# Performance work log

Measured on AMD Instinct MI355X. Metric: run time of the kernel, lower is better.

The kernel has to match this reference:

```python
import jax, jax.numpy as jnp
import numpy as np

N_USERS = 100000
N_ITEMS = 50000
N_TOPICS = 1000
N_NODES = N_USERS + N_ITEMS + N_TOPICS
DIM = 64
LAYERS = 3
NNZ = 4000000
BATCH = 16384


def setup_inputs() -> dict:
    key = jax.random.key(0)
    ks = jax.random.split(key, 8)
    user_w = jax.random.normal(ks[0], (N_USERS, DIM), dtype=jnp.float32) * 0.1
    item_w = jax.random.normal(ks[1], (N_ITEMS, DIM), dtype=jnp.float32) * 0.1
    topic_w = jax.random.normal(ks[2], (N_TOPICS, DIM), dtype=jnp.float32) * 0.1
    vals = jax.random.uniform(ks[3], (NNZ,), dtype=jnp.float32)
    row = jax.random.randint(ks[4], (NNZ,), 0, N_NODES, dtype=jnp.int32)
    col = jax.random.randint(ks[5], (NNZ,), 0, N_NODES, dtype=jnp.int32)
    users = jax.random.randint(ks[6], (BATCH,), 0, N_USERS, dtype=jnp.int32)
    items = jax.random.randint(ks[7], (BATCH,), 0, N_ITEMS, dtype=jnp.int32)
    return {"user_w": user_w, "item_w": item_w, "topic_w": topic_w,
            "vals": vals, "row": row, "col": col,
            "users": users, "items": items}


def _spmm(vals, row, col, x):
    # y[r] = sum over edges e with row[e]==r of vals[e] * x[col[e]]
    msgs = vals[:, None] * x[col]  # [NNZ, DIM]
    return jax.ops.segment_sum(msgs, row, num_segments=N_NODES)


def reference(user_w, item_w, topic_w, vals, row, col, users, items):
    all_emb = jnp.concatenate([user_w, item_w, topic_w], axis=0)  # [N, D]
    acc = all_emb
    emb = all_emb
    for _ in range(LAYERS):
        emb = _spmm(vals, row, col, emb)
        acc = acc + emb
    out = acc / jnp.asarray(LAYERS + 1, dtype=acc.dtype)  # mean over stacked layers
    u = out[users]                       # [B, D] user rows
    i = out[N_USERS + items]             # [B, D] item rows (offset into node table)
    return jnp.sum(u * i, axis=1)        # [B]
```

## Files before the change

kernel.cpp:

```cpp
#include <hip/hip_runtime.h>
#include <hip/hip_fp16.h>

#define N_USERS 100000
#define N_ITEMS 50000
#define N_TOPICS 1000
#define N_NODES (N_USERS + N_ITEMS + N_TOPICS)
#define DIM 64
#define NNZ 4000000
#define BATCH 16384

#define BROWS 128
#define NB ((N_NODES + BROWS - 1) / BROWS)
#define NPART 512
#define CHUNK ((NNZ + NPART - 1) / NPART)
#define SEGCAP 4608

#define QSCALE 16384.0f
#define QINV   6.103515625e-05f

__global__ void concat_init(const float4* __restrict__ uw,
                            const float4* __restrict__ iw,
                            const float4* __restrict__ tw,
                            __half2* __restrict__ x0) {
    int tid = blockIdx.x * blockDim.x + threadIdx.x;
    const int total = N_NODES * (DIM / 4);
    if (tid >= total) return;
    int node = tid >> 4;
    int q = tid & 15;
    float4 v;
    if (node < N_USERS)                v = uw[node * 16 + q];
    else if (node < N_USERS + N_ITEMS) v = iw[(node - N_USERS) * 16 + q];
    else                               v = tw[(node - N_USERS - N_ITEMS) * 16 + q];
    x0[tid * 2]     = __floats2half2_rn(v.x, v.y);
    x0[tid * 2 + 1] = __floats2half2_rn(v.z, v.w);
}

__global__ void __launch_bounds__(1024)
part_count(const int* __restrict__ row, int* __restrict__ hcnt) {
    __shared__ int h[NB];
    const int g = blockIdx.x;
    const int t = threadIdx.x;
    for (int i = t; i < NB; i += 1024) h[i] = 0;
    __syncthreads();
    int e0 = g * CHUNK;
    int e1 = e0 + CHUNK; if (e1 > NNZ) e1 = NNZ;
    for (int e = e0 + t; e < e1; e += 1024) {
        int r = __builtin_nontemporal_load(&row[e]);
        atomicAdd(&h[r >> 7], 1);
    }
    __syncthreads();
    int* dst = hcnt + (size_t)g * NB;
    for (int i = t; i < NB; i += 1024) dst[i] = h[i];
}

__global__ void part_scanA(int* __restrict__ hcnt, int* __restrict__ bcnt) {
    int b = blockIdx.x * 4 + (threadIdx.x >> 6);
    int lane = threadIdx.x & 63;
    if (b >= NB) return;
    int carry = 0;
    for (int base = 0; base < NPART; base += 64) {
        int g = base + lane;
        int v = hcnt[(size_t)g * NB + b];
        int x = v;
        #pragma unroll
        for (int off = 1; off < 64; off <<= 1) {
            int y = __shfl_up(x, off, 64);
            if (lane >= off) x += y;
        }
        int tot = __shfl(x, 63, 64);
        hcnt[(size_t)g * NB + b] = carry + x - v;
        carry += tot;
    }
    if (lane == 0) bcnt[b] = carry;
}

__global__ void part_scanB(const int* __restrict__ bcnt,
                           int* __restrict__ bptr,
                           int* __restrict__ rowptr) {
    __shared__ int wsum[16];
    __shared__ int carry_s;
    const int t = threadIdx.x;
    const int lane = t & 63;
    const int wid = t >> 6;
    if (t == 0) carry_s = 0;
    __syncthreads();
    for (int base = 0; base < NB; base += 1024) {
        int i = base + t;
        int v = (i < NB) ? bcnt[i] : 0;
        int x = v;
        #pragma unroll
        for (int off = 1; off < 64; off <<= 1) {
            int y = __shfl_up(x, off, 64);
            if (lane >= off) x += y;
        }
        if (lane == 63) wsum[wid] = x;
        __syncthreads();
        int wbase = 0;
        for (int w = 0; w < wid; ++w) wbase += wsum[w];
        int excl = carry_s + wbase + (x - v);
        if (i < NB) bptr[i] = excl;
        __syncthreads();
        if (t == 1023) carry_s = excl + v;
        __syncthreads();
    }
    if (t == 0) { bptr[NB] = NNZ; rowptr[N_NODES] = NNZ; }
}

__global__ void __launch_bounds__(1024)
part_scatter(const int* __restrict__ row,
             const int* __restrict__ col,
             const float* __restrict__ vals,
             const int* __restrict__ hcnt,
             const int* __restrict__ bptr,
             int2* __restrict__ cvtmp) {
    __shared__ int cur[NB];
    const int g = blockIdx.x;
    const int t = threadIdx.x;
    const int* hoff = hcnt + (size_t)g * NB;
    for (int i = t; i < NB; i += 1024) cur[i] = bptr[i] + hoff[i];
    __syncthreads();
    int e0 = g * CHUNK;
    int e1 = e0 + CHUNK; if (e1 > NNZ) e1 = NNZ;
    for (int e = e0 + t; e < e1; e += 1024) {
        int r = __builtin_nontemporal_load(&row[e]);
        int c = __builtin_nontemporal_load(&col[e]);
        float v = __builtin_nontemporal_load(&vals[e]);
        int p = atomicAdd(&cur[r >> 7], 1);
        cvtmp[p] = make_int2(((r & (BROWS - 1)) << 18) | c, __float_as_int(v));
    }
}

__global__ void __launch_bounds__(256)
bucket_sort(const int* __restrict__ bptr,
            const long long* __restrict__ cvtmp,
            unsigned int* __restrict__ cv,
            int* __restrict__ rowptr) {
    __shared__ int2 seg[SEGCAP];
    __shared__ int cnt[BROWS];
    __shared__ int cur[BROWS];
    const int t = threadIdx.x;
    const int b = blockIdx.x;
    const int beg = bptr[b];
    const int end = bptr[b + 1];
    const int n = end - beg;

    for (int i = t; i < BROWS; i += 256) cnt[i] = 0;
    const bool lds_path = (n <= SEGCAP);

    if (lds_path) {
        for (int j = t; j < n; j += 256) {
            long long e = __builtin_nontemporal_load(&cvtmp[beg + j]);
            seg[j] = make_int2((int)e, (int)(e >> 32));
        }
    }
    __syncthreads();

    if (lds_path) {
        for (int j = t; j < n; j += 256)
            atomicAdd(&cnt[(seg[j].x >> 18) & (BROWS - 1)], 1);
    } else {
        for (int j = beg + t; j < end; j += 256) {
            long long e = cvtmp[j];
            atomicAdd(&cnt[((int)e >> 18) & (BROWS - 1)], 1);
        }
    }
    __syncthreads();

    if (t < 64) {
        int lane = t;
        int v0 = cnt[lane];
        int v1 = cnt[64 + lane];
        int x0 = v0;
        #pragma unroll
        for (int off = 1; off < 64; off <<= 1) {
            int y = __shfl_up(x0, off, 64);
            if (lane >= off) x0 += y;
        }
        int tot0 = __shfl(x0, 63, 64);
        int x1 = v1;
        #pragma unroll
        for (int off = 1; off < 64; off <<= 1) {
            int y = __shfl_up(x1, off, 64);
            if (lane >= off) x1 += y;
        }
        x1 += tot0;
        int e0 = x0 - v0;
        int e1 = x1 - v1;
        cur[lane] = e0;
        cur[64 + lane] = e1;
        int rowbase = b * BROWS;
        if (rowbase + lane < N_NODES)      rowptr[rowbase + lane] = beg + e0;
        if (rowbase + 64 + lane < N_NODES) rowptr[rowbase + 64 + lane] = beg + e1;
    }
    __syncthreads();

    if (lds_path) {
        for (int j = t; j < n; j += 256) {
            int2 e = seg[j];
            int p = atomicAdd(&cur[(e.x >> 18) & (BROWS - 1)], 1);
            float v = __int_as_float(e.y);
            unsigned int qv = (unsigned int)(v * QSCALE + 0.5f);
            if (qv > 16383u) qv = 16383u;
            cv[beg + p] = (qv << 18) | (unsigned int)(e.x & 0x3FFFF);
        }
    } else {
        for (int j = beg + t; j < end; j += 256) {
            long long e = cvtmp[j];
            int lo = (int)e;
            float v = __int_as_float((int)(e >> 32));
            int p = atomicAdd(&cur[(lo >> 18) & (BROWS - 1)], 1);
            unsigned int qv = (unsigned int)(v * QSCALE + 0.5f);
            if (qv > 16383u) qv = 16383u;
            cv[beg + p] = (qv << 18) | (unsigned int)(lo & 0x3FFFF);
        }
    }
}

__global__ void spmm_csr(const int* __restrict__ rowptr,
                         const unsigned int* __restrict__ cv,
                         const __half2* __restrict__ x2,
                         __half2* __restrict__ y2) {
    int blk = blockIdx.x;
    int bucket = (blk >> 8) * 8 + (blk & 7);
    int sub = (blk & 255) >> 3;
    int r = bucket * BROWS + sub * 4 + (threadIdx.x >> 6);
    if (r >= N_NODES) return;
    int lane = threadIdx.x & 63;
    int half = lane >> 5;
    int d = lane & 31;
    int beg = rowptr[r];
    int end = rowptr[r + 1];
    int mid = beg + ((end - beg + 1) >> 1);
    int j    = half ? mid : beg;
    int jend = half ? end : mid;
    float ax0 = 0.0f, ay0 = 0.0f, ax1 = 0.0f, ay1 = 0.0f;
    for (; j + 7 < jend; j += 8) {
        unsigned int u[8];
        __half2 h[8];
        #pragma unroll
        for (int k = 0; k < 8; ++k) u[k] = __builtin_nontemporal_load(&cv[j + k]);
        #pragma unroll
        for (int k = 0; k < 8; ++k) h[k] = x2[(size_t)(u[k] & 0x3FFFF) * 32 + d];
        #pragma unroll
        for (int k = 0; k < 8; k += 2) {
            float2 f0 = __half22float2(h[k]);
            float2 f1 = __half22float2(h[k + 1]);
            float v0 = (float)(u[k] >> 18) * QINV;
            float v1 = (float)(u[k + 1] >> 18) * QINV;
            ax0 = fmaf(v0, f0.x, ax0); ay0 = fmaf(v0, f0.y, ay0);
            ax1 = fmaf(v1, f1.x, ax1); ay1 = fmaf(v1, f1.y, ay1);
        }
    }
    for (; j + 3 < jend; j += 4) {
        unsigned int u0 = __builtin_nontemporal_load(&cv[j]);
        unsigned int u1 = __builtin_nontemporal_load(&cv[j + 1]);
        unsigned int u2 = __builtin_nontemporal_load(&cv[j + 2]);
        unsigned int u3 = __builtin_nontemporal_load(&cv[j + 3]);
        float2 f0 = __half22float2(x2[(size_t)(u0 & 0x3FFFF) * 32 + d]);
        float2 f1 = __half22float2(x2[(size_t)(u1 & 0x3FFFF) * 32 + d]);
        float2 f2 = __half22float2(x2[(size_t)(u2 & 0x3FFFF) * 32 + d]);
        float2 f3 = __half22float2(x2[(size_t)(u3 & 0x3FFFF) * 32 + d]);
        float v0 = (float)(u0 >> 18) * QINV;
        float v1 = (float)(u1 >> 18) * QINV;
        float v2 = (float)(u2 >> 18) * QINV;
        float v3 = (float)(u3 >> 18) * QINV;
        ax0 = fmaf(v0, f0.x, ax0); ay0 = fmaf(v0, f0.y, ay0);
        ax1 = fmaf(v1, f1.x, ax1); ay1 = fmaf(v1, f1.y, ay1);
        ax0 = fmaf(v2, f2.x, ax0); ay0 = fmaf(v2, f2.y, ay0);
        ax1 = fmaf(v3, f3.x, ax1); ay1 = fmaf(v3, f3.y, ay1);
    }
    for (; j < jend; ++j) {
        unsigned int u = __builtin_nontemporal_load(&cv[j]);
        float2 f = __half22float2(x2[(size_t)(u & 0x3FFFF) * 32 + d]);
        float v = (float)(u >> 18) * QINV;
        ax0 = fmaf(v, f.x, ax0); ay0 = fmaf(v, f.y, ay0);
    }
    float ax = ax0 + ax1;
    float ay = ay0 + ay1;
    ax += __shfl_down(ax, 32, 64);
    ay += __shfl_down(ay, 32, 64);
    if (lane < 32) y2[(size_t)r * 32 + d] = __floats2half2_rn(ax, ay);
}

__global__ void spmm_batch(const int* __restrict__ rowptr,
                           const unsigned int* __restrict__ cv,
                           const __half2* __restrict__ x2,
                           const int* __restrict__ users,
                           const int* __restrict__ items,
                           float* __restrict__ accb) {
    int b = blockIdx.x * 4 + (threadIdx.x >> 6);
    if (b >= 2 * BATCH) return;
    int lane = threadIdx.x & 63;
    int half = lane >> 5;
    int d = lane & 31;
    int r = (b < BATCH) ? users[b] : (N_USERS + items[b - BATCH]);
    int beg = rowptr[r];
    int end = rowptr[r + 1];
    int mid = beg + ((end - beg + 1) >> 1);
    int j    = half ? mid : beg;
    int jend = half ? end : mid;
    float ax0 = 0.0f, ay0 = 0.0f, ax1 = 0.0f, ay1 = 0.0f;
    for (; j + 7 < jend; j += 8) {
        unsigned int u[8];
        __half2 h[8];
        #pragma unroll
        for (int k = 0; k < 8; ++k) u[k] = __builtin_nontemporal_load(&cv[j + k]);
        #pragma unroll
        for (int k = 0; k < 8; ++k) h[k] = x2[(size_t)(u[k] & 0x3FFFF) * 32 + d];
        #pragma unroll
        for (int k = 0; k < 8; k += 2) {
            float2 f0 = __half22float2(h[k]);
            float2 f1 = __half22float2(h[k + 1]);
            float v0 = (float)(u[k] >> 18) * QINV;
            float v1 = (float)(u[k + 1] >> 18) * QINV;
            ax0 = fmaf(v0, f0.x, ax0); ay0 = fmaf(v0, f0.y, ay0);
            ax1 = fmaf(v1, f1.x, ax1); ay1 = fmaf(v1, f1.y, ay1);
        }
    }
    for (; j + 3 < jend; j += 4) {
        unsigned int u0 = __builtin_nontemporal_load(&cv[j]);
        unsigned int u1 = __builtin_nontemporal_load(&cv[j + 1]);
        unsigned int u2 = __builtin_nontemporal_load(&cv[j + 2]);
        unsigned int u3 = __builtin_nontemporal_load(&cv[j + 3]);
        float2 f0 = __half22float2(x2[(size_t)(u0 & 0x3FFFF) * 32 + d]);
        float2 f1 = __half22float2(x2[(size_t)(u1 & 0x3FFFF) * 32 + d]);
        float2 f2 = __half22float2(x2[(size_t)(u2 & 0x3FFFF) * 32 + d]);
        float2 f3 = __half22float2(x2[(size_t)(u3 & 0x3FFFF) * 32 + d]);
        float v0 = (float)(u0 >> 18) * QINV;
        float v1 = (float)(u1 >> 18) * QINV;
        float v2 = (float)(u2 >> 18) * QINV;
        float v3 = (float)(u3 >> 18) * QINV;
        ax0 = fmaf(v0, f0.x, ax0); ay0 = fmaf(v0, f0.y, ay0);
        ax1 = fmaf(v1, f1.x, ax1); ay1 = fmaf(v1, f1.y, ay1);
        ax0 = fmaf(v2, f2.x, ax0); ay0 = fmaf(v2, f2.y, ay0);
        ax1 = fmaf(v3, f3.x, ax1); ay1 = fmaf(v3, f3.y, ay1);
    }
    for (; j < jend; ++j) {
        unsigned int u = __builtin_nontemporal_load(&cv[j]);
        float2 f = __half22float2(x2[(size_t)(u & 0x3FFFF) * 32 + d]);
        float v = (float)(u >> 18) * QINV;
        ax0 = fmaf(v, f.x, ax0); ay0 = fmaf(v, f.y, ay0);
    }
    float ax = ax0 + ax1;
    float ay = ay0 + ay1;
    ax += __shfl_down(ax, 32, 64);
    ay += __shfl_down(ay, 32, 64);
    if (lane < 32) {
        float2* a2 = (float2*)(accb + (size_t)b * 64 + 2 * d);
        float2 o = *a2;
        o.x += ax; o.y += ay;
        *a2 = o;
    }
}

__global__ void batch_init(const float4* __restrict__ uw,
                           const float4* __restrict__ iw,
                           const int* __restrict__ users,
                           const int* __restrict__ items,
                           float4* __restrict__ accb) {
    int tid = blockIdx.x * blockDim.x + threadIdx.x;
    const int total = 2 * BATCH * (DIM / 4);
    if (tid >= total) return;
    int r = tid >> 4;
    int q = tid & 15;
    float4 v;
    if (r < BATCH) v = uw[(size_t)users[r] * 16 + q];
    else           v = iw[(size_t)items[r - BATCH] * 16 + q];
    accb[tid] = v;
}

__global__ void batch_add(const __half* __restrict__ emb,
                          const int* __restrict__ users,
                          const int* __restrict__ items,
                          float4* __restrict__ accb) {
    int tid = blockIdx.x * blockDim.x + threadIdx.x;
    const int total = 2 * BATCH * (DIM / 4);
    if (tid >= total) return;
    int r = tid >> 4;
    int q = tid & 15;
    int node = (r < BATCH) ? users[r] : (N_USERS + items[r - BATCH]);
    const __half2* e2 = (const __half2*)(emb + (size_t)node * 64 + q * 4);
    float2 lo = __half22float2(e2[0]);
    float2 hi = __half22float2(e2[1]);
    float4 a = accb[tid];
    a.x += lo.x; a.y += lo.y; a.z += hi.x; a.w += hi.y;
    accb[tid] = a;
}

__global__ void final_dot(const float* __restrict__ accb,
                          float* __restrict__ out) {
    int b = blockIdx.x * 4 + (threadIdx.x >> 6);
    int lane = threadIdx.x & 63;
    if (b >= BATCH) return;
    float pu = accb[(size_t)b * 64 + lane];
    float pi = accb[(size_t)(BATCH + b) * 64 + lane];
    float p = pu * pi;
    #pragma unroll
    for (int off = 32; off > 0; off >>= 1)
        p += __shfl_down(p, off, 64);
    if (lane == 0) out[b] = p * (1.0f / 16.0f);
}

extern "C" void kernel_launch(void* const* d_in, const int* in_sizes, int n_in,
                              void* d_out, int out_size, void* d_ws, size_t ws_size,
                              hipStream_t stream) {
    const float* uw   = (const float*)d_in[0];
    const float* iw   = (const float*)d_in[1];
    const float* tw   = (const float*)d_in[2];
    const float* vals = (const float*)d_in[3];
    const int*   row  = (const int*)d_in[4];
    const int*   col  = (const int*)d_in[5];
    const int*   users= (const int*)d_in[6];
    const int*   items= (const int*)d_in[7];
    float* out = (float*)d_out;

    char* ws = (char*)d_ws;
    const size_t NODE_F = (size_t)N_NODES * DIM;
    __half* A     = (__half*)ws; ws += NODE_F * 2;
    __half* B     = (__half*)ws; ws += NODE_F * 2;
    float* ACCB   = (float*)ws;  ws += (size_t)2 * BATCH * DIM * 4;
    int*   bcnt   = (int*)ws;    ws += (size_t)NB * 4;
    int*   bptr   = (int*)ws;    ws += (size_t)(NB + 1) * 4;
    int*   rowptr = (int*)ws;    ws += (size_t)(N_NODES + 1) * 4;
    int*   hcnt   = (int*)ws;    ws += (size_t)NPART * NB * 4;
    unsigned int* cv = (unsigned int*)ws; ws += (size_t)NNZ * 4;
    int2*  cvtmp  = (int2*)ws;   ws += (size_t)NNZ * 8;

    const int node_v4  = N_NODES * (DIM / 4);
    const int batch_v4 = 2 * BATCH * (DIM / 4);

    concat_init<<<(node_v4 + 255) / 256, 256, 0, stream>>>(
        (const float4*)uw, (const float4*)iw, (const float4*)tw, (__half2*)A);
    batch_init<<<(batch_v4 + 255) / 256, 256, 0, stream>>>(
        (const float4*)uw, (const float4*)iw, users, items, (float4*)ACCB);

    part_count<<<NPART, 1024, 0, stream>>>(row, hcnt);
    part_scanA<<<(NB + 3) / 4, 256, 0, stream>>>(hcnt, bcnt);
    part_scanB<<<1, 1024, 0, stream>>>(bcnt, bptr, rowptr);
    part_scatter<<<NPART, 1024, 0, stream>>>(row, col, vals, hcnt, bptr, cvtmp);
    bucket_sort<<<NB, 256, 0, stream>>>(bptr, (const long long*)cvtmp, cv, rowptr);

    const int spmm_blocks = ((NB + 7) / 8) * 256;
    spmm_csr<<<spmm_blocks, 256, 0, stream>>>(rowptr, cv, (const __half2*)A,
                                              (__half2*)B);
    batch_add<<<(batch_v4 + 255) / 256, 256, 0, stream>>>(
        B, users, items, (float4*)ACCB);
    spmm_csr<<<spmm_blocks, 256, 0, stream>>>(rowptr, cv, (const __half2*)B,
                                              (__half2*)A);
    batch_add<<<(batch_v4 + 255) / 256, 256, 0, stream>>>(
        A, users, items, (float4*)ACCB);
    spmm_batch<<<(2 * BATCH + 3) / 4, 256, 0, stream>>>(
        rowptr, cv, (const __half2*)A, users, items, ACCB);

    final_dot<<<(BATCH + 3) / 4, 256, 0, stream>>>(ACCB, out);
}
```

Baseline: 473.4 us.

## Split embeddings into two 32-dim planes and run SpMM per plane

```diff
diff --git a/kernel.cpp b/kernel.cpp
--- a/kernel.cpp
+++ b/kernel.cpp
@@ -17,6 +17,8 @@
 
 #define QSCALE 16384.0f
 #define QINV   6.103515625e-05f
+
+#define PSTRIDE ((size_t)N_NODES * 16)
 
 __global__ void concat_init(const float4* __restrict__ uw,
                             const float4* __restrict__ iw,
@@ -31,8 +33,11 @@
     if (node < N_USERS)                v = uw[node * 16 + q];
     else if (node < N_USERS + N_ITEMS) v = iw[(node - N_USERS) * 16 + q];
     else                               v = tw[(node - N_USERS - N_ITEMS) * 16 + q];
-    x0[tid * 2]     = __floats2half2_rn(v.x, v.y);
-    x0[tid * 2 + 1] = __floats2half2_rn(v.z, v.w);
+    int plane = q >> 3;
+    int dq = q & 7;
+    __half2* dst = x0 + ((size_t)plane * N_NODES + node) * 16 + dq * 2;
+    dst[0] = __floats2half2_rn(v.x, v.y);
+    dst[1] = __floats2half2_rn(v.z, v.w);
 }
 
 __global__ void __launch_bounds__(1024)
@@ -218,135 +223,140 @@
 
 __global__ void spmm_csr(const int* __restrict__ rowptr,
                          const unsigned int* __restrict__ cv,
-                         const __half2* __restrict__ x2,
-                         __half2* __restrict__ y2) {
+                         const __half2* __restrict__ xp,
+                         __half2* __restrict__ yp) {
     int blk = blockIdx.x;
     int bucket = (blk >> 8) * 8 + (blk & 7);
     int sub = (blk & 255) >> 3;
     int r = bucket * BROWS + sub * 4 + (threadIdx.x >> 6);
     if (r >= N_NODES) return;
     int lane = threadIdx.x & 63;
-    int half = lane >> 5;
-    int d = lane & 31;
+    int qt = lane >> 4;
+    int d = lane & 15;
     int beg = rowptr[r];
-    int end = rowptr[r + 1];
-    int mid = beg + ((end - beg + 1) >> 1);
-    int j    = half ? mid : beg;
-    int jend = half ? end : mid;
-    float ax0 = 0.0f, ay0 = 0.0f, ax1 = 0.0f, ay1 = 0.0f;
-    for (; j + 7 < jend; j += 8) {
+    int n = rowptr[r + 1] - beg;
+    const unsigned int* cvb = cv + beg;
+    float ax = 0.0f, ay = 0.0f;
+    int base = 0;
+    for (; base + 32 <= n; base += 32) {
         unsigned int u[8];
         __half2 h[8];
         #pragma unroll
-        for (int k = 0; k < 8; ++k) u[k] = __builtin_nontemporal_load(&cv[j + k]);
-        #pragma unroll
-        for (int k = 0; k < 8; ++k) h[k] = x2[(size_t)(u[k] & 0x3FFFF) * 32 + d];
-        #pragma unroll
-        for (int k = 0; k < 8; k += 2) {
-            float2 f0 = __half22float2(h[k]);
-            float2 f1 = __half22float2(h[k + 1]);
-            float v0 = (float)(u[k] >> 18) * QINV;
-            float v1 = (float)(u[k + 1] >> 18) * QINV;
-            ax0 = fmaf(v0, f0.x, ax0); ay0 = fmaf(v0, f0.y, ay0);
-            ax1 = fmaf(v1, f1.x, ax1); ay1 = fmaf(v1, f1.y, ay1);
-        }
-    }
-    for (; j + 3 < jend; j += 4) {
-        unsigned int u0 = __builtin_nontemporal_load(&cv[j]);
-        unsigned int u1 = __builtin_nontemporal_load(&cv[j + 1]);
-        unsigned int u2 = __builtin_nontemporal_load(&cv[j + 2]);
-        unsigned int u3 = __builtin_nontemporal_load(&cv[j + 3]);
-        float2 f0 = __half22float2(x2[(size_t)(u0 & 0x3FFFF) * 32 + d]);
-        float2 f1 = __half22float2(x2[(size_t)(u1 & 0x3FFFF) * 32 + d]);
-        float2 f2 = __half22float2(x2[(size_t)(u2 & 0x3FFFF) * 32 + d]);
-        float2 f3 = __half22float2(x2[(size_t)(u3 & 0x3FFFF) * 32 + d]);
-        float v0 = (float)(u0 >> 18) * QINV;
-        float v1 = (float)(u1 >> 18) * QINV;
-        float v2 = (float)(u2 >> 18) * QINV;
-        float v3 = (float)(u3 >> 18) * QINV;
-        ax0 = fmaf(v0, f0.x, ax0); ay0 = fmaf(v0, f0.y, ay0);
-        ax1 = fmaf(v1, f1.x, ax1); ay1 = fmaf(v1, f1.y, ay1);
-        ax0 = fmaf(v2, f2.x, ax0); ay0 = fmaf(v2, f2.y, ay0);
-        ax1 = fmaf(v3, f3.x, ax1); ay1 = fmaf(v3, f3.y, ay1);
-    }
-    for (; j < jend; ++j) {
-        unsigned int u = __builtin_nontemporal_load(&cv[j]);
-        float2 f = __half22float2(x2[(size_t)(u & 0x3FFFF) * 32 + d]);
+        for (int k = 0; k < 8; ++k) u[k] = cvb[base + qt + 4 * k];
+        #pragma unroll
+        for (int k = 0; k < 8; ++k) h[k] = xp[(size_t)(u[k] & 0x3FFFF) * 16 + d];
+        #pragma unroll
+        for (int k = 0; k < 8; ++k) {
+            float2 f = __half22float2(h[k]);
+            float v = (float)(u[k] >> 18) * QINV;
+            ax = fmaf(v, f.x, ax); ay = fmaf(v, f.y, ay);
+        }
+    }
+    for (; base + 16 <= n; base += 16) {
+        unsigned int u[4];
+        __half2 h[4];
+        #pragma unroll
+        for (int k = 0; k < 4; ++k) u[k] = cvb[base + qt + 4 * k];
+        #pragma unroll
+        for (int k = 0; k < 4; ++k) h[k] = xp[(size_t)(u[k] & 0x3FFFF) * 16 + d];
+        #pragma unroll
+        for (int k = 0; k < 4; ++k) {
+            float2 f = __half22float2(h[k]);
+            float v = (float)(u[k] >> 18) * QINV;
+            ax = fmaf(v, f.x, ax); ay = fmaf(v, f.y, ay);
+        }
+    }
+    for (; base + 4 <= n; base += 4) {
+        unsigned int u = cvb[base + qt];
+        float2 f = __half22float2(xp[(size_t)(u & 0x3FFFF) * 16 + d]);
         float v = (float)(u >> 18) * QINV;
-        ax0 = fmaf(v, f.x, ax0); ay0 = fmaf(v, f.y, ay0);
-    }
-    float ax = ax0 + ax1;
-    float ay = ay0 + ay1;
+        ax = fmaf(v, f.x, ax); ay = fmaf(v, f.y, ay);
+    }
+    int rem = n - base;
+    if (qt < rem) {
+        unsigned int u = cvb[base + qt];
+        float2 f = __half22float2(xp[(size_t)(u & 0x3FFFF) * 16 + d]);
+        float v = (float)(u >> 18) * QINV;
+        ax = fmaf(v, f.x, ax); ay = fmaf(v, f.y, ay);
+    }
+    ax += __shfl_down(ax, 16, 64);
+    ay += __shfl_down(ay, 16, 64);
     ax += __shfl_down(ax, 32, 64);
     ay += __shfl_down(ay, 32, 64);
-    if (lane < 32) y2[(size_t)r * 32 + d] = __floats2half2_rn(ax, ay);
+    if (lane < 16) {
+        __half2 o = __floats2half2_rn(ax, ay);
+        unsigned int ob;
+        __builtin_memcpy(&ob, &o, 4);
+        __builtin_nontemporal_store(ob,
+            (unsigned int*)&yp[(size_t)r * 16 + d]);
+    }
 }
 
 __global__ void spmm_batch(const int* __restrict__ rowptr,
                            const unsigned int* __restrict__ cv,
-                           const __half2* __restrict__ x2,
+                           const __half2* __restrict__ xp,
                            const int* __restrict__ users,
                            const int* __restrict__ items,
-                           float* __restrict__ accb) {
+                           float* __restrict__ accb,
+                           int plane) {
     int b = blockIdx.x * 4 + (threadIdx.x >> 6);
     if (b >= 2 * BATCH) return;
     int lane = threadIdx.x & 63;
-    int half = lane >> 5;
-    int d = lane & 31;
+    int qt = lane >> 4;
+    int d = lane & 15;
     int r = (b < BATCH) ? users[b] : (N_USERS + items[b - BATCH]);
     int beg = rowptr[r];
-    int end = rowptr[r + 1];
-    int mid = beg + ((end - beg + 1) >> 1);
-    int j    = half ? mid : beg;
-    int jend = half ? end : mid;
-    float ax0 = 0.0f, ay0 = 0.0f, ax1 = 0.0f, ay1 = 0.0f;
-    for (; j + 7 < jend; j += 8) {
+    int n = rowptr[r + 1] - beg;
+    const unsigned int* cvb = cv + beg;
+    float ax = 0.0f, ay = 0.0f;
+    int base = 0;
+    for (; base + 32 <= n; base += 32) {
         unsigned int u[8];
         __half2 h[8];
         #pragma unroll
-        for (int k = 0; k < 8; ++k) u[k] = __builtin_nontemporal_load(&cv[j + k]);
-        #pragma unroll
-        for (int k = 0; k < 8; ++k) h[k] = x2[(size_t)(u[k] & 0x3FFFF) * 32 + d];
-        #pragma unroll
-        for (int k = 0; k < 8; k += 2) {
-            float2 f0 = __half22float2(h[k]);
-            float2 f1 = __half22float2(h[k + 1]);
-            float v0 = (float)(u[k] >> 18) * QINV;
-            float v1 = (float)(u[k + 1] >> 18) * QINV;
-            ax0 = fmaf(v0, f0.x, ax0); ay0 = fmaf(v0, f0.y, ay0);
-            ax1 = fmaf(v1, f1.x, ax1); ay1 = fmaf(v1, f1.y, ay1);
-        }
-    }
-    for (; j + 3 < jend; j += 4) {
-        unsigned int u0 = __builtin_nontemporal_load(&cv[j]);
-        unsigned int u1 = __builtin_nontemporal_load(&cv[j + 1]);
-        unsigned int u2 = __builtin_nontemporal_load(&cv[j + 2]);
-        unsigned int u3 = __builtin_nontemporal_load(&cv[j + 3]);
-        float2 f0 = __half22float2(x2[(size_t)(u0 & 0x3FFFF) * 32 + d]);
-        float2 f1 = __half22float2(x2[(size_t)(u1 & 0x3FFFF) * 32 + d]);
-        float2 f2 = __half22float2(x2[(size_t)(u2 & 0x3FFFF) * 32 + d]);
-        float2 f3 = __half22float2(x2[(size_t)(u3 & 0x3FFFF) * 32 + d]);
-        float v0 = (float)(u0 >> 18) * QINV;
-        float v1 = (float)(u1 >> 18) * QINV;
-        float v2 = (float)(u2 >> 18) * QINV;
-        float v3 = (float)(u3 >> 18) * QINV;
-        ax0 = fmaf(v0, f0.x, ax0); ay0 = fmaf(v0, f0.y, ay0);
-        ax1 = fmaf(v1, f1.x, ax1); ay1 = fmaf(v1, f1.y, ay1);
-        ax0 = fmaf(v2, f2.x, ax0); ay0 = fmaf(v2, f2.y, ay0);
-        ax1 = fmaf(v3, f3.x, ax1); ay1 = fmaf(v3, f3.y, ay1);
-    }
-    for (; j < jend; ++j) {
-        unsigned int u = __builtin_nontemporal_load(&cv[j]);
-        float2 f = __half22float2(x2[(size_t)(u & 0x3FFFF) * 32 + d]);
+        for (int k = 0; k < 8; ++k) u[k] = cvb[base + qt + 4 * k];
+        #pragma unroll
+        for (int k = 0; k < 8; ++k) h[k] = xp[(size_t)(u[k] & 0x3FFFF) * 16 + d];
+        #pragma unroll
+        for (int k = 0; k < 8; ++k) {
+            float2 f = __half22float2(h[k]);
+            float v = (float)(u[k] >> 18) * QINV;
+            ax = fmaf(v, f.x, ax); ay = fmaf(v, f.y, ay);
+        }
+    }
+    for (; base + 16 <= n; base += 16) {
+        unsigned int u[4];
+        __half2 h[4];
+        #pragma unroll
+        for (int k = 0; k < 4; ++k) u[k] = cvb[base + qt + 4 * k];
+        #pragma unroll
+        for (int k = 0; k < 4; ++k) h[k] = xp[(size_t)(u[k] & 0x3FFFF) * 16 + d];
+        #pragma unroll
+        for (int k = 0; k < 4; ++k) {
+            float2 f = __half22float2(h[k]);
+            float v = (float)(u[k] >> 18) * QINV;
+            ax = fmaf(v, f.x, ax); ay = fmaf(v, f.y, ay);
+        }
+    }
+    for (; base + 4 <= n; base += 4) {
+        unsigned int u = cvb[base + qt];
+        float2 f = __half22float2(xp[(size_t)(u & 0x3FFFF) * 16 + d]);
         float v = (float)(u >> 18) * QINV;
-        ax0 = fmaf(v, f.x, ax0); ay0 = fmaf(v, f.y, ay0);
-    }
-    float ax = ax0 + ax1;
-    float ay = ay0 + ay1;
+        ax = fmaf(v, f.x, ax); ay = fmaf(v, f.y, ay);
+    }
+    int rem = n - base;
+    if (qt < rem) {
+        unsigned int u = cvb[base + qt];
+        float2 f = __half22float2(xp[(size_t)(u & 0x3FFFF) * 16 + d]);
+        float v = (float)(u >> 18) * QINV;
+        ax = fmaf(v, f.x, ax); ay = fmaf(v, f.y, ay);
+    }
+    ax += __shfl_down(ax, 16, 64);
+    ay += __shfl_down(ay, 16, 64);
     ax += __shfl_down(ax, 32, 64);
     ay += __shfl_down(ay, 32, 64);
-    if (lane < 32) {
-        float2* a2 = (float2*)(accb + (size_t)b * 64 + 2 * d);
+    if (lane < 16) {
+        float2* a2 = (float2*)(accb + (size_t)b * 64 + plane * 32 + 2 * d);
         float2 o = *a2;
         o.x += ax; o.y += ay;
         *a2 = o;
@@ -369,7 +379,7 @@
     accb[tid] = v;
 }
 
-__global__ void batch_add(const __half* __restrict__ emb,
+__global__ void batch_add(const __half2* __restrict__ emb2,
                           const int* __restrict__ users,
                           const int* __restrict__ items,
                           float4* __restrict__ accb) {
@@ -379,7 +389,9 @@
     int r = tid >> 4;
     int q = tid & 15;
     int node = (r < BATCH) ? users[r] : (N_USERS + items[r - BATCH]);
-    const __half2* e2 = (const __half2*)(emb + (size_t)node * 64 + q * 4);
+    int plane = q >> 3;
+    int dq = q & 7;
+    const __half2* e2 = emb2 + ((size_t)plane * N_NODES + node) * 16 + dq * 2;
     float2 lo = __half22float2(e2[0]);
     float2 hi = __half22float2(e2[1]);
     float4 a = accb[tid];
@@ -429,8 +441,11 @@
     const int node_v4  = N_NODES * (DIM / 4);
     const int batch_v4 = 2 * BATCH * (DIM / 4);
 
+    __half2* A2 = (__half2*)A;
+    __half2* B2 = (__half2*)B;
+
     concat_init<<<(node_v4 + 255) / 256, 256, 0, stream>>>(
-        (const float4*)uw, (const float4*)iw, (const float4*)tw, (__half2*)A);
+        (const float4*)uw, (const float4*)iw, (const float4*)tw, A2);
     batch_init<<<(batch_v4 + 255) / 256, 256, 0, stream>>>(
         (const float4*)uw, (const float4*)iw, users, items, (float4*)ACCB);
 
@@ -441,16 +456,18 @@
     bucket_sort<<<NB, 256, 0, stream>>>(bptr, (const long long*)cvtmp, cv, rowptr);
 
     const int spmm_blocks = ((NB + 7) / 8) * 256;
-    spmm_csr<<<spmm_blocks, 256, 0, stream>>>(rowptr, cv, (const __half2*)A,
-                                              (__half2*)B);
+    spmm_csr<<<spmm_blocks, 256, 0, stream>>>(rowptr, cv, A2, B2);
+    spmm_csr<<<spmm_blocks, 256, 0, stream>>>(rowptr, cv, A2 + PSTRIDE, B2 + PSTRIDE);
     batch_add<<<(batch_v4 + 255) / 256, 256, 0, stream>>>(
-        B, users, items, (float4*)ACCB);
-    spmm_csr<<<spmm_blocks, 256, 0, stream>>>(rowptr, cv, (const __half2*)B,
-                                              (__half2*)A);
+        B2, users, items, (float4*)ACCB);
+    spmm_csr<<<spmm_blocks, 256, 0, stream>>>(rowptr, cv, B2, A2);
+    spmm_csr<<<spmm_blocks, 256, 0, stream>>>(rowptr, cv, B2 + PSTRIDE, A2 + PSTRIDE);
     batch_add<<<(batch_v4 + 255) / 256, 256, 0, stream>>>(
-        A, users, items, (float4*)ACCB);
+        A2, users, items, (float4*)ACCB);
     spmm_batch<<<(2 * BATCH + 3) / 4, 256, 0, stream>>>(
-        rowptr, cv, (const __half2*)A, users, items, ACCB);
+        rowptr, cv, A2, users, items, ACCB, 0);
+    spmm_batch<<<(2 * BATCH + 3) / 4, 256, 0, stream>>>(
+        rowptr, cv, A2 + PSTRIDE, users, items, ACCB, 1);
 
     final_dot<<<(BATCH + 3) / 4, 256, 0, stream>>>(ACCB, out);
 }
```

After: 574.4 us. +21.3%, slower.

## Interleave edge split across half-waves, use cached index loads, nontemporal output stores

Applied to the files above, without the earlier changes.

```diff
diff --git a/kernel.cpp b/kernel.cpp
--- a/kernel.cpp
+++ b/kernel.cpp
@@ -11,7 +11,7 @@
 
 #define BROWS 128
 #define NB ((N_NODES + BROWS - 1) / BROWS)
-#define NPART 512
+#define NPART 256
 #define CHUNK ((NNZ + NPART - 1) / NPART)
 #define SEGCAP 4608
 
@@ -230,15 +230,13 @@
     int d = lane & 31;
     int beg = rowptr[r];
     int end = rowptr[r + 1];
-    int mid = beg + ((end - beg + 1) >> 1);
-    int j    = half ? mid : beg;
-    int jend = half ? end : mid;
     float ax0 = 0.0f, ay0 = 0.0f, ax1 = 0.0f, ay1 = 0.0f;
-    for (; j + 7 < jend; j += 8) {
+    int j = beg + half;
+    for (; j + 14 < end; j += 16) {
         unsigned int u[8];
         __half2 h[8];
         #pragma unroll
-        for (int k = 0; k < 8; ++k) u[k] = __builtin_nontemporal_load(&cv[j + k]);
+        for (int k = 0; k < 8; ++k) u[k] = cv[j + 2 * k];
         #pragma unroll
         for (int k = 0; k < 8; ++k) h[k] = x2[(size_t)(u[k] & 0x3FFFF) * 32 + d];
         #pragma unroll
@@ -251,11 +249,11 @@
             ax1 = fmaf(v1, f1.x, ax1); ay1 = fmaf(v1, f1.y, ay1);
         }
     }
-    for (; j + 3 < jend; j += 4) {
-        unsigned int u0 = __builtin_nontemporal_load(&cv[j]);
-        unsigned int u1 = __builtin_nontemporal_load(&cv[j + 1]);
-        unsigned int u2 = __builtin_nontemporal_load(&cv[j + 2]);
-        unsigned int u3 = __builtin_nontemporal_load(&cv[j + 3]);
+    for (; j + 6 < end; j += 8) {
+        unsigned int u0 = cv[j];
+        unsigned int u1 = cv[j + 2];
+        unsigned int u2 = cv[j + 4];
+        unsigned int u3 = cv[j + 6];
         float2 f0 = __half22float2(x2[(size_t)(u0 & 0x3FFFF) * 32 + d]);
         float2 f1 = __half22float2(x2[(size_t)(u1 & 0x3FFFF) * 32 + d]);
         float2 f2 = __half22float2(x2[(size_t)(u2 & 0x3FFFF) * 32 + d]);
@@ -269,8 +267,8 @@
         ax0 = fmaf(v2, f2.x, ax0); ay0 = fmaf(v2, f2.y, ay0);
         ax1 = fmaf(v3, f3.x, ax1); ay1 = fmaf(v3, f3.y, ay1);
     }
-    for (; j < jend; ++j) {
-        unsigned int u = __builtin_nontemporal_load(&cv[j]);
+    for (; j < end; j += 2) {
+        unsigned int u = cv[j];
         float2 f = __half22float2(x2[(size_t)(u & 0x3FFFF) * 32 + d]);
         float v = (float)(u >> 18) * QINV;
         ax0 = fmaf(v, f.x, ax0); ay0 = fmaf(v, f.y, ay0);
@@ -279,7 +277,12 @@
     float ay = ay0 + ay1;
     ax += __shfl_down(ax, 32, 64);
     ay += __shfl_down(ay, 32, 64);
-    if (lane < 32) y2[(size_t)r * 32 + d] = __floats2half2_rn(ax, ay);
+    if (lane < 32) {
+        __half2 o = __floats2half2_rn(ax, ay);
+        unsigned int ob;
+        __builtin_memcpy(&ob, &o, 4);
+        __builtin_nontemporal_store(ob, (unsigned int*)&y2[(size_t)r * 32 + d]);
+    }
 }
 
 __global__ void spmm_batch(const int* __restrict__ rowptr,
@@ -296,15 +299,13 @@
     int r = (b < BATCH) ? users[b] : (N_USERS + items[b - BATCH]);
     int beg = rowptr[r];
     int end = rowptr[r + 1];
-    int mid = beg + ((end - beg + 1) >> 1);
-    int j    = half ? mid : beg;
-    int jend = half ? end : mid;
     float ax0 = 0.0f, ay0 = 0.0f, ax1 = 0.0f, ay1 = 0.0f;
-    for (; j + 7 < jend; j += 8) {
+    int j = beg + half;
+    for (; j + 14 < end; j += 16) {
         unsigned int u[8];
         __half2 h[8];
         #pragma unroll
-        for (int k = 0; k < 8; ++k) u[k] = __builtin_nontemporal_load(&cv[j + k]);
+        for (int k = 0; k < 8; ++k) u[k] = cv[j + 2 * k];
         #pragma unroll
         for (int k = 0; k < 8; ++k) h[k] = x2[(size_t)(u[k] & 0x3FFFF) * 32 + d];
         #pragma unroll
@@ -317,11 +318,11 @@
             ax1 = fmaf(v1, f1.x, ax1); ay1 = fmaf(v1, f1.y, ay1);
         }
     }
-    for (; j + 3 < jend; j += 4) {
-        unsigned int u0 = __builtin_nontemporal_load(&cv[j]);
-        unsigned int u1 = __builtin_nontemporal_load(&cv[j + 1]);
-        unsigned int u2 = __builtin_nontemporal_load(&cv[j + 2]);
-        unsigned int u3 = __builtin_nontemporal_load(&cv[j + 3]);
+    for (; j + 6 < end; j += 8) {
+        unsigned int u0 = cv[j];
+        unsigned int u1 = cv[j + 2];
+        unsigned int u2 = cv[j + 4];
+        unsigned int u3 = cv[j + 6];
         float2 f0 = __half22float2(x2[(size_t)(u0 & 0x3FFFF) * 32 + d]);
         float2 f1 = __half22float2(x2[(size_t)(u1 & 0x3FFFF) * 32 + d]);
         float2 f2 = __half22float2(x2[(size_t)(u2 & 0x3FFFF) * 32 + d]);
@@ -335,8 +336,8 @@
         ax0 = fmaf(v2, f2.x, ax0); ay0 = fmaf(v2, f2.y, ay0);
         ax1 = fmaf(v3, f3.x, ax1); ay1 = fmaf(v3, f3.y, ay1);
     }
-    for (; j < jend; ++j) {
-        unsigned int u = __builtin_nontemporal_load(&cv[j]);
+    for (; j < end; j += 2) {
+        unsigned int u = cv[j];
         float2 f = __half22float2(x2[(size_t)(u & 0x3FFFF) * 32 + d]);
         float v = (float)(u >> 18) * QINV;
         ax0 = fmaf(v, f.x, ax0); ay0 = fmaf(v, f.y, ay0);
```

Result: faster. 442.7 us (-6.5%).
